# Performance work log

Measured on AMD Instinct MI355X. Metric: run time of the kernel, lower is better.

## Reference

```python
import jax, jax.numpy as jnp
import numpy as np

B, S, DIM, H = 8, 1024, 1024, 16
HID = 512  # FeedForward default hidden_dim=512 (module passes only dim)
DH = DIM // H
EPS = 1e-5


def setup_inputs() -> dict:
    key = jax.random.key(0)
    ks = jax.random.split(key, 12)
    s = 1.0 / np.sqrt(DIM)
    return {
        "x": jax.random.normal(ks[0], (B, S, DIM), dtype=jnp.float32),
        "Wq": jax.random.normal(ks[1], (DIM, DIM), dtype=jnp.float32) * s,
        "Wk": jax.random.normal(ks[2], (DIM, DIM), dtype=jnp.float32) * s,
        "Wv": jax.random.normal(ks[3], (DIM, DIM), dtype=jnp.float32) * s,
        "Wo": jax.random.normal(ks[4], (DIM, DIM), dtype=jnp.float32) * s,
        "ln1_g": jnp.ones((DIM,), jnp.float32),
        "ln1_b": jnp.zeros((DIM,), jnp.float32),
        "W1": jax.random.normal(ks[5], (DIM, HID), dtype=jnp.float32) * s,
        "b1": jnp.zeros((HID,), jnp.float32),
        "W2": jax.random.normal(ks[6], (HID, DIM), dtype=jnp.float32) * (1.0 / np.sqrt(HID)),
        "b2": jnp.zeros((DIM,), jnp.float32),
        "ln2_g": jnp.ones((DIM,), jnp.float32),
        "ln2_b": jnp.zeros((DIM,), jnp.float32),
    }


def _layer_norm(x, g, b):
    mu = jnp.mean(x, axis=-1, keepdims=True)
    var = jnp.mean(jnp.square(x - mu), axis=-1, keepdims=True)
    return (x - mu) * jax.lax.rsqrt(var + EPS) * g + b


def reference(x, Wq, Wk, Wv, Wo, ln1_g, ln1_b, W1, b1, W2, b2, ln2_g, ln2_b):
    # Multi-head self-attention (dropout = identity at eval)
    def heads(t):  # [B,S,DIM] -> [B,H,S,DH]
        return t.reshape(B, S, H, DH).transpose(0, 2, 1, 3)

    q = heads(x @ Wq)
    k = heads(x @ Wk)
    v = heads(x @ Wv)
    scores = jnp.einsum("bhqd,bhkd->bhqk", q, k) / jnp.sqrt(jnp.float32(DH))
    attn = jax.nn.softmax(scores, axis=-1)
    ctx = jnp.einsum("bhqk,bhkd->bhqd", attn, v)
    ctx = ctx.transpose(0, 2, 1, 3).reshape(B, S, DIM)
    mha = ctx @ Wo

    h = _layer_norm(mha + x, ln1_g, ln1_b)
    ff = jax.nn.relu(h @ W1 + b1) @ W2 + b2
    out = _layer_norm(ff + h, ln2_g, ln2_b)
    return out
```

## Files before the change

### kernel.cpp

```cpp
#include <hip/hip_runtime.h>
#include <cstdint>
#include <cstddef>

#define DEV __device__ __forceinline__

typedef __bf16 bf16x8 __attribute__((ext_vector_type(8)));
typedef __bf16 bf16x4 __attribute__((ext_vector_type(4)));
typedef short  short4v __attribute__((ext_vector_type(4)));
typedef float  f32x4  __attribute__((ext_vector_type(4)));

static constexpr int Bb  = 8;
static constexpr int S   = 1024;
static constexpr int DIM = 1024;
static constexpr int H   = 16;
static constexpr int DH  = 64;
static constexpr int HID = 512;
static constexpr int M   = Bb * S;

DEV uint16_t f2bf(float f) {
  union { float f; uint32_t u; } v; v.f = f;
  uint32_t r = v.u + 0x7fffu + ((v.u >> 16) & 1u);
  return (uint16_t)(r >> 16);
}
DEV float bf2f(uint32_t u) {
  union { uint32_t u; float f; } v; v.u = u << 16;
  return v.f;
}

DEV void gl_lds16(const uint16_t* g, uint16_t* lds) {
  __builtin_amdgcn_global_load_lds(
      (const __attribute__((address_space(1))) void*)g,
      (__attribute__((address_space(3))) void*)lds, 16, 0, 0);
}

DEV bf16x8 ld8(const uint16_t* p) { return *reinterpret_cast<const bf16x8*>(p); }

#if __has_builtin(__builtin_amdgcn_mfma_f32_16x16x16bf16_1k)
DEV f32x4 mfma16(bf16x4 a, bf16x4 b, f32x4 c) {
  return __builtin_amdgcn_mfma_f32_16x16x16bf16_1k(
      __builtin_bit_cast(short4v, a), __builtin_bit_cast(short4v, b), c, 0, 0, 0);
}
#else
DEV f32x4 mfma16(bf16x4 a, bf16x4 b, f32x4 c) {
  asm volatile("v_mfma_f32_16x16x16_bf16 %0, %1, %2, %0" : "+v"(c) : "v"(a), "v"(b));
  return c;
}
#endif

DEV int swz(int row, int col) {
  return row * 64 + (((col >> 3) ^ (row & 7)) << 3) + (col & 7);
}

__global__ __launch_bounds__(256) void prep_all(const float* __restrict__ x,
                                                uint16_t* __restrict__ x16,
                                                const float* __restrict__ Wq,
                                                const float* __restrict__ Wk,
                                                const float* __restrict__ Wv,
                                                const float* __restrict__ Wo,
                                                const float* __restrict__ W1,
                                                const float* __restrict__ W2,
                                                uint16_t* __restrict__ wqkv_t,
                                                uint16_t* __restrict__ wo_t,
                                                uint16_t* __restrict__ w1_t,
                                                uint16_t* __restrict__ w2_t) {
  int bid = blockIdx.x;
  int tid = threadIdx.x;
  if (bid < 4096) {
    int i = (bid * 256 + tid) * 8;
    const float4* p = reinterpret_cast<const float4*>(x + i);
    float4 a = p[0], b = p[1];
    uint4 pk;
    pk.x = (uint32_t)f2bf(a.x) | ((uint32_t)f2bf(a.y) << 16);
    pk.y = (uint32_t)f2bf(a.z) | ((uint32_t)f2bf(a.w) << 16);
    pk.z = (uint32_t)f2bf(b.x) | ((uint32_t)f2bf(b.y) << 16);
    pk.w = (uint32_t)f2bf(b.z) | ((uint32_t)f2bf(b.w) << 16);
    *reinterpret_cast<uint4*>(x16 + i) = pk;
    return;
  }
  bid -= 4096;
  const float* src;
  uint16_t* dst;
  int R, C, bx, by;
  if (bid < 4096) {
    int which = bid >> 10, id = bid & 1023;
    if (which == 0)      { src = Wq; dst = wqkv_t; }
    else if (which == 1) { src = Wk; dst = wqkv_t + 1048576; }
    else if (which == 2) { src = Wv; dst = wqkv_t + 2097152; }
    else                 { src = Wo; dst = wo_t; }
    R = 1024; C = 1024; bx = id & 31; by = id >> 5;
  } else if (bid < 4608) {
    int id = bid - 4096;
    src = W1; dst = w1_t; R = 1024; C = 512; bx = id & 15; by = id >> 4;
  } else {
    int id = bid - 4608;
    src = W2; dst = w2_t; R = 512; C = 1024; bx = id & 31; by = id >> 5;
  }
  __shared__ float tile[32][33];
  int c0 = bx * 32, r0 = by * 32;
  int tx = tid & 31, ty = tid >> 5;
  #pragma unroll
  for (int i = 0; i < 4; i++)
    tile[ty + i * 8][tx] = src[(size_t)(r0 + ty + i * 8) * C + c0 + tx];
  __syncthreads();
  #pragma unroll
  for (int i = 0; i < 4; i++)
    dst[(size_t)(c0 + ty + i * 8) * R + r0 + tx] = f2bf(tile[tx][ty + i * 8]);
}

__global__ __launch_bounds__(256) void vtrans(const uint16_t* __restrict__ qkv,
                                              uint16_t* __restrict__ vt) {
  int bh = blockIdx.x;
  int s0 = blockIdx.y * 64;
  int b = bh >> 4, h = bh & 15;
  int tid = threadIdx.x;
  __shared__ uint16_t t[64][65];
  #pragma unroll
  for (int j = 0; j < 16; j++) {
    int lin = j * 256 + tid;
    int sl = lin >> 6, d = lin & 63;
    t[d][sl] = qkv[(size_t)(b * S + s0 + sl) * 3072 + 2048 + h * 64 + d];
  }
  __syncthreads();
  #pragma unroll
  for (int j = 0; j < 16; j++) {
    int lin = j * 256 + tid;
    int dl = lin >> 6, sl = lin & 63;
    vt[((size_t)bh * 64 + dl) * S + s0 + sl] = t[dl][sl];
  }
}

template <int BIAS, int RELU, int OUT_BF16>
__global__ __launch_bounds__(256) void gemm_bt(const uint16_t* __restrict__ A,
                                               const uint16_t* __restrict__ Bt,
                                               const float* __restrict__ bias,
                                               void* __restrict__ Cout,
                                               int Mm, int N, int K) {
  __shared__ __align__(16) uint16_t As[128 * 32];
  __shared__ __align__(16) uint16_t Bs[128 * 32];
  const int tid = threadIdx.x;
  const int w = tid >> 6, l = tid & 63;
  int nwg = gridDim.x * gridDim.y;
  int lin = blockIdx.y * gridDim.x + blockIdx.x;
  if (!(nwg & 7)) lin = (lin & 7) * (nwg >> 3) + (lin >> 3);
  const int bx = lin % gridDim.x, by = lin / gridDim.x;
  const int m0 = by * 128, n0 = bx * 128;
  const int wr = (w >> 1) * 64, wc = (w & 1) * 64;
  const int wbase = w * 64;
  f32x4 acc[4][4] = {};
  const uint16_t* Ag = A + (size_t)m0 * K;
  const uint16_t* Bg = Bt + (size_t)n0 * K;

  for (int k0 = 0; k0 < K; k0 += 32) {
    __syncthreads();
    #pragma unroll
    for (int n = 0; n < 2; n++) {
      int lin2 = n * 256 + tid;
      int row = lin2 >> 2, col = (lin2 & 3) * 8;
      gl_lds16(Ag + (size_t)row * K + k0 + col, &As[(size_t)(n * 256 + wbase) * 8]);
      gl_lds16(Bg + (size_t)row * K + k0 + col, &Bs[(size_t)(n * 256 + wbase) * 8]);
    }
    __syncthreads();
    bf16x8 af[4], bfr[4];
    #pragma unroll
    for (int i = 0; i < 4; i++) {
      af[i]  = ld8(&As[(wr + i * 16 + (l & 15)) * 32 + (l >> 4) * 8]);
      bfr[i] = ld8(&Bs[(wc + i * 16 + (l & 15)) * 32 + (l >> 4) * 8]);
    }
    #pragma unroll
    for (int i = 0; i < 4; i++)
      #pragma unroll
      for (int j = 0; j < 4; j++)
        acc[i][j] = __builtin_amdgcn_mfma_f32_16x16x32_bf16(af[i], bfr[j], acc[i][j], 0, 0, 0);
  }

  const int r0 = m0 + wr + (l >> 4) * 4;
  const int c0 = n0 + wc + (l & 15);
  #pragma unroll
  for (int j = 0; j < 4; j++) {
    int col = c0 + j * 16;
    float bv = BIAS ? bias[col] : 0.0f;
    #pragma unroll
    for (int i = 0; i < 4; i++) {
      #pragma unroll
      for (int r = 0; r < 4; r++) {
        float v = acc[i][j][r] + bv;
        if (RELU) v = fmaxf(v, 0.0f);
        int row = r0 + i * 16 + r;
        if (OUT_BF16)
          ((uint16_t*)Cout)[(size_t)row * N + col] = f2bf(v);
        else
          ((float*)Cout)[(size_t)row * N + col] = v;
      }
    }
  }
}

__global__ __launch_bounds__(512, 2) void gemm256(const uint16_t* __restrict__ A,
                                                  const uint16_t* __restrict__ Bt,
                                                  uint16_t* __restrict__ Cout,
                                                  int N, int K) {
  __shared__ __align__(16) uint16_t As[2][256 * 64];
  __shared__ __align__(16) uint16_t Bs[2][256 * 64];
  const int tid = threadIdx.x;
  const int w = tid >> 6, l = tid & 63;
  const int hi = l >> 4, c = l & 15;
  int nwg = gridDim.x * gridDim.y;
  int lin = blockIdx.y * gridDim.x + blockIdx.x;
  if (!(nwg & 7)) lin = (lin & 7) * (nwg >> 3) + (lin >> 3);
  const int bx = lin % gridDim.x, by = lin / gridDim.x;
  const int m0 = by * 256, n0 = bx * 256;
  const int wr = w >> 2, wc = w & 3;
  const uint16_t* Ag = A + (size_t)m0 * K;
  const uint16_t* Bg = Bt + (size_t)n0 * K;
  f32x4 acc[8][4] = {};

  const int srow = tid >> 3, sch = tid & 7;
  auto stage = [&](int k0, int buf) {
    #pragma unroll
    for (int i = 0; i < 4; i++) {
      int row = i * 64 + srow;
      int scol = (sch ^ (row & 7)) * 8;
      gl_lds16(Ag + (size_t)row * K + k0 + scol, &As[buf][(i * 512 + w * 64) * 8]);
    }
    #pragma unroll
    for (int i = 0; i < 4; i++) {
      int row = i * 64 + srow;
      int scol = (sch ^ (row & 7)) * 8;
      gl_lds16(Bg + (size_t)row * K + k0 + scol, &Bs[buf][(i * 512 + w * 64) * 8]);
    }
  };

  stage(0, 0);
  stage(64, 1);
  asm volatile("s_waitcnt vmcnt(8)" ::: "memory");
  __builtin_amdgcn_s_barrier();

  const int NTK = K >> 6;
  for (int t = 0; t < NTK; t++) {
    const int cur = t & 1;
    const uint16_t* Ab = As[cur];
    const uint16_t* Bb = Bs[cur];
    bf16x8 bfr[4][2];
    #pragma unroll
    for (int ni = 0; ni < 4; ni++)
      #pragma unroll
      for (int kk = 0; kk < 2; kk++)
        bfr[ni][kk] = ld8(&Bb[swz(wc * 64 + ni * 16 + c, kk * 32 + hi * 8)]);
    #pragma unroll
    for (int mi = 0; mi < 8; mi++) {
      bf16x8 a0 = ld8(&Ab[swz(wr * 128 + mi * 16 + c, hi * 8)]);
      bf16x8 a1 = ld8(&Ab[swz(wr * 128 + mi * 16 + c, 32 + hi * 8)]);
      #pragma unroll
      for (int ni = 0; ni < 4; ni++) {
        acc[mi][ni] = __builtin_amdgcn_mfma_f32_16x16x32_bf16(a0, bfr[ni][0], acc[mi][ni], 0, 0, 0);
        acc[mi][ni] = __builtin_amdgcn_mfma_f32_16x16x32_bf16(a1, bfr[ni][1], acc[mi][ni], 0, 0, 0);
      }
    }
    if (t == NTK - 1) break;
    asm volatile("s_waitcnt lgkmcnt(0)" ::: "memory");
    __builtin_amdgcn_s_barrier();
    if (t + 2 < NTK) {
      stage((t + 2) << 6, cur);
      asm volatile("s_waitcnt vmcnt(8)" ::: "memory");
    } else {
      asm volatile("s_waitcnt vmcnt(0)" ::: "memory");
    }
    __builtin_amdgcn_s_barrier();
  }

  const int r0 = m0 + wr * 128 + hi * 4;
  const int c0 = n0 + wc * 64 + c;
  #pragma unroll
  for (int mi = 0; mi < 8; mi++)
    #pragma unroll
    for (int ni = 0; ni < 4; ni++)
      #pragma unroll
      for (int r = 0; r < 4; r++)
        Cout[(size_t)(r0 + mi * 16 + r) * N + c0 + ni * 16] = f2bf(acc[mi][ni][r]);
}

__global__ __launch_bounds__(256, 4) void attn8(const uint16_t* __restrict__ qkv,
                                                const uint16_t* __restrict__ vt,
                                                uint16_t* __restrict__ ctx) {
  int blk = blockIdx.x;
  int xcd = blk & 7, idx = blk >> 3;
  int qt = idx & 7;
  int bh = xcd + 8 * (idx >> 3);
  int h = bh & 15, b = bh >> 4;
  int q0 = qt * 128;
  int tid = threadIdx.x;
  int w = tid >> 6, l = tid & 63;
  int hi = l >> 4, c = l & 15;

  __shared__ __align__(16) uint16_t Klds[2][64 * 64];
  __shared__ __align__(16) uint16_t Vlds[2][64 * 64];

  const uint16_t* qbase = qkv + (size_t)(b * S + q0 + w * 32) * 3072 + h * 64;
  bf16x8 aq[2][2];
  #pragma unroll
  for (int qg = 0; qg < 2; qg++)
    #pragma unroll
    for (int dk = 0; dk < 2; dk++)
      aq[qg][dk] = ld8(qbase + (size_t)(qg * 16 + c) * 3072 + dk * 32 + hi * 8);

  f32x4 acc[2][4] = {};
  float psum[2] = {};

  const uint16_t* kgbase = qkv + (size_t)(b * S) * 3072 + 1024 + h * 64;
  const uint16_t* vgbase = vt + (size_t)(b * 16 + h) * 64 * S;

  int srow = tid >> 3, sch = tid & 7;
  uint4 kreg[2], vreg[2];

  auto load_tiles = [&](int kt) {
    #pragma unroll
    for (int i = 0; i < 2; i++) {
      int row = srow + i * 32;
      kreg[i] = *(const uint4*)(kgbase + (size_t)(kt + row) * 3072 + sch * 8);
      vreg[i] = *(const uint4*)(vgbase + (size_t)row * S + kt + sch * 8);
    }
  };
  auto store_tiles = [&](int buf) {
    #pragma unroll
    for (int i = 0; i < 2; i++) {
      int row = srow + i * 32;
      *(uint4*)&Klds[buf][swz(row, sch * 8)] = kreg[i];
      *(uint4*)&Vlds[buf][swz(row, sch * 8)] = vreg[i];
    }
  };

  load_tiles(0);
  store_tiles(0);
  __syncthreads();

  constexpr float C2 = 0.125f * 1.44269504f;
  constexpr int NT = S / 64;
  for (int t = 0; t < NT; t++) {
    int cur = t & 1;
    if (t + 1 < NT) load_tiles((t + 1) * 64);

    #pragma unroll
    for (int kb = 0; kb < 4; kb++) {
      bf16x8 kf0 = ld8(&Klds[cur][swz(kb * 16 + c, hi * 8)]);
      bf16x8 kf1 = ld8(&Klds[cur][swz(kb * 16 + c, 32 + hi * 8)]);
      bf16x4 pb[2];
      #pragma unroll
      for (int qg = 0; qg < 2; qg++) {
        f32x4 z = {0.f, 0.f, 0.f, 0.f};
        z = __builtin_amdgcn_mfma_f32_16x16x32_bf16(kf0, aq[qg][0], z, 0, 0, 0);
        z = __builtin_amdgcn_mfma_f32_16x16x32_bf16(kf1, aq[qg][1], z, 0, 0, 0);
        #pragma unroll
        for (int r = 0; r < 4; r++) {
          float p = exp2f(z[r] * C2);
          psum[qg] += p;
          pb[qg][r] = (__bf16)p;
        }
      }
      #pragma unroll
      for (int db = 0; db < 4; db++) {
        bf16x4 va = *(const bf16x4*)&Vlds[cur][swz(db * 16 + c, kb * 16 + hi * 4)];
        acc[0][db] = mfma16(va, pb[0], acc[0][db]);
        acc[1][db] = mfma16(va, pb[1], acc[1][db]);
      }
    }

    if (t + 1 < NT) store_tiles(cur ^ 1);
    __syncthreads();
  }

  #pragma unroll
  for (int qg = 0; qg < 2; qg++) {
    psum[qg] += __shfl_xor(psum[qg], 16);
    psum[qg] += __shfl_xor(psum[qg], 32);
  }

  uint16_t* Bw = &Vlds[w >> 1][(w & 1) * 2048];
  #pragma unroll
  for (int qg = 0; qg < 2; qg++) {
    float inv = 1.0f / psum[qg];
    int q = qg * 16 + c;
    #pragma unroll
    for (int db = 0; db < 4; db++) {
      uint2 pk;
      pk.x = (uint32_t)f2bf(acc[qg][db][0] * inv) |
             ((uint32_t)f2bf(acc[qg][db][1] * inv) << 16);
      pk.y = (uint32_t)f2bf(acc[qg][db][2] * inv) |
             ((uint32_t)f2bf(acc[qg][db][3] * inv) << 16);
      int chunk4 = (db * 4 + hi) ^ (q & 15);
      *(uint2*)&Bw[q * 64 + chunk4 * 4] = pk;
    }
  }
  int rrow = l >> 3, rch = l & 7;
  size_t gq0 = (size_t)(b * S + q0 + w * 32);
  #pragma unroll
  for (int it = 0; it < 4; it++) {
    int row = it * 8 + rrow;
    int k0 = (2 * rch) ^ (row & 15);
    int base = (k0 & ~1) * 4;
    uint4 v = *(const uint4*)&Bw[row * 64 + base];
    if (row & 1) { uint32_t t0 = v.x, t1 = v.y; v.x = v.z; v.y = v.w; v.z = t0; v.w = t1; }
    *(uint4*)&ctx[(gq0 + row) * DIM + h * 64 + rch * 8] = v;
  }
}

__global__ __launch_bounds__(256) void ln1_b(const uint16_t* __restrict__ a16,
                                             const uint16_t* __restrict__ x16,
                                             const float* __restrict__ g,
                                             const float* __restrict__ beta,
                                             uint16_t* __restrict__ h16) {
  int row = blockIdx.x;
  int t = threadIdx.x;
  int w = t >> 6, l = t & 63;
  uint2 av = reinterpret_cast<const uint2*>(a16 + (size_t)row * DIM)[t];
  uint2 xv = reinterpret_cast<const uint2*>(x16 + (size_t)row * DIM)[t];
  float v0 = bf2f(av.x & 0xffff) + bf2f(xv.x & 0xffff);
  float v1 = bf2f(av.x >> 16)    + bf2f(xv.x >> 16);
  float v2 = bf2f(av.y & 0xffff) + bf2f(xv.y & 0xffff);
  float v3 = bf2f(av.y >> 16)    + bf2f(xv.y >> 16);
  float s = v0 + v1 + v2 + v3;
  float sq = v0 * v0 + v1 * v1 + v2 * v2 + v3 * v3;
  #pragma unroll
  for (int off = 32; off >= 1; off >>= 1) {
    s += __shfl_xor(s, off);
    sq += __shfl_xor(sq, off);
  }
  __shared__ float ws[4], wq[4];
  if (l == 0) { ws[w] = s; wq[w] = sq; }
  __syncthreads();
  s = ws[0] + ws[1] + ws[2] + ws[3];
  sq = wq[0] + wq[1] + wq[2] + wq[3];
  float mu = s * (1.0f / DIM);
  float var = sq * (1.0f / DIM) - mu * mu;
  float rstd = rsqrtf(var + 1e-5f);
  const float4 gv = reinterpret_cast<const float4*>(g)[t];
  const float4 btv = reinterpret_cast<const float4*>(beta)[t];
  float o0 = (v0 - mu) * rstd * gv.x + btv.x;
  float o1 = (v1 - mu) * rstd * gv.y + btv.y;
  float o2 = (v2 - mu) * rstd * gv.z + btv.z;
  float o3 = (v3 - mu) * rstd * gv.w + btv.w;
  uint2 pk;
  pk.x = (uint32_t)f2bf(o0) | ((uint32_t)f2bf(o1) << 16);
  pk.y = (uint32_t)f2bf(o2) | ((uint32_t)f2bf(o3) << 16);
  reinterpret_cast<uint2*>(h16 + (size_t)row * DIM)[t] = pk;
}

__global__ __launch_bounds__(256) void ln2_b(const uint16_t* __restrict__ ff16,
                                             const uint16_t* __restrict__ h16,
                                             const float* __restrict__ g,
                                             const float* __restrict__ beta,
                                             float* __restrict__ out_f) {
  int row = blockIdx.x;
  int t = threadIdx.x;
  int w = t >> 6, l = t & 63;
  uint2 av = reinterpret_cast<const uint2*>(ff16 + (size_t)row * DIM)[t];
  uint2 hv = reinterpret_cast<const uint2*>(h16 + (size_t)row * DIM)[t];
  float v0 = bf2f(av.x & 0xffff) + bf2f(hv.x & 0xffff);
  float v1 = bf2f(av.x >> 16)    + bf2f(hv.x >> 16);
  float v2 = bf2f(av.y & 0xffff) + bf2f(hv.y & 0xffff);
  float v3 = bf2f(av.y >> 16)    + bf2f(hv.y >> 16);
  float s = v0 + v1 + v2 + v3;
  float sq = v0 * v0 + v1 * v1 + v2 * v2 + v3 * v3;
  #pragma unroll
  for (int off = 32; off >= 1; off >>= 1) {
    s += __shfl_xor(s, off);
    sq += __shfl_xor(sq, off);
  }
  __shared__ float ws[4], wq[4];
  if (l == 0) { ws[w] = s; wq[w] = sq; }
  __syncthreads();
  s = ws[0] + ws[1] + ws[2] + ws[3];
  sq = wq[0] + wq[1] + wq[2] + wq[3];
  float mu = s * (1.0f / DIM);
  float var = sq * (1.0f / DIM) - mu * mu;
  float rstd = rsqrtf(var + 1e-5f);
  const float4 gv = reinterpret_cast<const float4*>(g)[t];
  const float4 btv = reinterpret_cast<const float4*>(beta)[t];
  float4 o;
  o.x = (v0 - mu) * rstd * gv.x + btv.x;
  o.y = (v1 - mu) * rstd * gv.y + btv.y;
  o.z = (v2 - mu) * rstd * gv.z + btv.z;
  o.w = (v3 - mu) * rstd * gv.w + btv.w;
  reinterpret_cast<float4*>(out_f + (size_t)row * DIM)[t] = o;
}

extern "C" void kernel_launch(void* const* d_in, const int* in_sizes, int n_in,
                              void* d_out, int out_size, void* d_ws, size_t ws_size,
                              hipStream_t stream) {
  const float* x    = (const float*)d_in[0];
  const float* Wq   = (const float*)d_in[1];
  const float* Wk   = (const float*)d_in[2];
  const float* Wv   = (const float*)d_in[3];
  const float* Wo   = (const float*)d_in[4];
  const float* ln1g = (const float*)d_in[5];
  const float* ln1b = (const float*)d_in[6];
  const float* W1   = (const float*)d_in[7];
  const float* b1   = (const float*)d_in[8];
  const float* W2   = (const float*)d_in[9];
  const float* b2   = (const float*)d_in[10];
  const float* ln2g = (const float*)d_in[11];
  const float* ln2b = (const float*)d_in[12];
  float* out = (float*)d_out;

  char* ws = (char*)d_ws;
  uint16_t* wqkv_t = (uint16_t*)(ws + 0);
  uint16_t* wo_t   = (uint16_t*)(ws + 6291456);
  uint16_t* w1_t   = (uint16_t*)(ws + 8388608);
  uint16_t* w2_t   = (uint16_t*)(ws + 9437184);
  uint16_t* x16    = (uint16_t*)(ws + 10485760);
  uint16_t* qkv16  = (uint16_t*)(ws + 27262976);
  uint16_t* mha16  = (uint16_t*)(ws + 27262976);
  uint16_t* ff16   = (uint16_t*)(ws + 27262976);
  uint16_t* h16    = (uint16_t*)(ws + 60817408);
  uint16_t* vt16   = (uint16_t*)(ws + 77594624);
  uint16_t* mid16  = vt16;
  uint16_t* ctx16  = (uint16_t*)(ws + 94371840);

  prep_all<<<9216, 256, 0, stream>>>(x, x16, Wq, Wk, Wv, Wo, W1, W2,
                                     wqkv_t, wo_t, w1_t, w2_t);
  gemm256<<<dim3(12, 32), 512, 0, stream>>>(x16, wqkv_t, qkv16, 3072, DIM);
  vtrans<<<dim3(128, 16), 256, 0, stream>>>(qkv16, vt16);
  attn8<<<1024, 256, 0, stream>>>(qkv16, vt16, ctx16);
  gemm_bt<0, 0, 1><<<dim3(8, 64), 256, 0, stream>>>(ctx16, wo_t, nullptr, mha16, M, DIM, DIM);
  ln1_b<<<M, 256, 0, stream>>>(mha16, x16, ln1g, ln1b, h16);
  gemm_bt<1, 1, 1><<<dim3(4, 64), 256, 0, stream>>>(h16, w1_t, b1, mid16, M, HID, DIM);
  gemm_bt<1, 0, 1><<<dim3(8, 64), 256, 0, stream>>>(mid16, w2_t, b2, ff16, M, DIM, HID);
  ln2_b<<<M, 256, 0, stream>>>(ff16, h16, ln2g, ln2b, out);
}
```

Baseline: 262.4 us.

## Fuse V transpose into QKV GEMM epilogue and stage attention tiles directly to LDS

The QKV GEMM epilogue now writes the V columns straight into a per-head transposed layout (vt), which removes the separate vtrans kernel and its extra read and write of V. The attention kernel switches from register-staged K/V loads plus LDS stores to direct global-to-LDS loads (gl_lds16) with an XOR column swizzle, then waits on vmcnt before each barrier. This saves one launch, V memory traffic and VGPR pressure. In exchange the transposed stores are narrower and strided, and waiting for the loads at the end of each iteration may reduce the overlap between loads and compute.

```diff
diff --git a/kernel.cpp b/kernel.cpp
--- a/kernel.cpp
+++ b/kernel.cpp
@@ -107,28 +107,6 @@
     dst[(size_t)(c0 + ty + i * 8) * R + r0 + tx] = f2bf(tile[tx][ty + i * 8]);
 }
 
-__global__ __launch_bounds__(256) void vtrans(const uint16_t* __restrict__ qkv,
-                                              uint16_t* __restrict__ vt) {
-  int bh = blockIdx.x;
-  int s0 = blockIdx.y * 64;
-  int b = bh >> 4, h = bh & 15;
-  int tid = threadIdx.x;
-  __shared__ uint16_t t[64][65];
-  #pragma unroll
-  for (int j = 0; j < 16; j++) {
-    int lin = j * 256 + tid;
-    int sl = lin >> 6, d = lin & 63;
-    t[d][sl] = qkv[(size_t)(b * S + s0 + sl) * 3072 + 2048 + h * 64 + d];
-  }
-  __syncthreads();
-  #pragma unroll
-  for (int j = 0; j < 16; j++) {
-    int lin = j * 256 + tid;
-    int dl = lin >> 6, sl = lin & 63;
-    vt[((size_t)bh * 64 + dl) * S + s0 + sl] = t[dl][sl];
-  }
-}
-
 template <int BIAS, int RELU, int OUT_BF16>
 __global__ __launch_bounds__(256) void gemm_bt(const uint16_t* __restrict__ A,
                                                const uint16_t* __restrict__ Bt,
@@ -198,6 +176,7 @@
 __global__ __launch_bounds__(512, 2) void gemm256(const uint16_t* __restrict__ A,
                                                   const uint16_t* __restrict__ Bt,
                                                   uint16_t* __restrict__ Cout,
+                                                  uint16_t* __restrict__ vt,
                                                   int N, int K) {
   __shared__ __align__(16) uint16_t As[2][256 * 64];
   __shared__ __align__(16) uint16_t Bs[2][256 * 64];
@@ -270,16 +249,32 @@
 
   const int r0 = m0 + wr * 128 + hi * 4;
   const int c0 = n0 + wc * 64 + c;
-  #pragma unroll
-  for (int mi = 0; mi < 8; mi++)
-    #pragma unroll
-    for (int ni = 0; ni < 4; ni++)
-      #pragma unroll
-      for (int r = 0; r < 4; r++)
-        Cout[(size_t)(r0 + mi * 16 + r) * N + c0 + ni * 16] = f2bf(acc[mi][ni][r]);
-}
-
-__global__ __launch_bounds__(256, 4) void attn8(const uint16_t* __restrict__ qkv,
+  if (c0 >= 2048) {
+    #pragma unroll
+    for (int ni = 0; ni < 4; ni++) {
+      int hd = c0 + ni * 16 - 2048;
+      #pragma unroll
+      for (int mi = 0; mi < 8; mi++) {
+        int row = r0 + mi * 16;
+        size_t vi = ((size_t)(row >> 10) * 1024 + hd) * 1024 + (row & 1023);
+        uint2 pk;
+        pk.x = (uint32_t)f2bf(acc[mi][ni][0]) | ((uint32_t)f2bf(acc[mi][ni][1]) << 16);
+        pk.y = (uint32_t)f2bf(acc[mi][ni][2]) | ((uint32_t)f2bf(acc[mi][ni][3]) << 16);
+        *(uint2*)&vt[vi] = pk;
+      }
+    }
+  } else {
+    #pragma unroll
+    for (int mi = 0; mi < 8; mi++)
+      #pragma unroll
+      for (int ni = 0; ni < 4; ni++)
+        #pragma unroll
+        for (int r = 0; r < 4; r++)
+          Cout[(size_t)(r0 + mi * 16 + r) * N + c0 + ni * 16] = f2bf(acc[mi][ni][r]);
+  }
+}
+
+__global__ __launch_bounds__(256, 4) void attn9(const uint16_t* __restrict__ qkv,
                                                 const uint16_t* __restrict__ vt,
                                                 uint16_t* __restrict__ ctx) {
   int blk = blockIdx.x;
@@ -309,35 +304,28 @@
   const uint16_t* kgbase = qkv + (size_t)(b * S) * 3072 + 1024 + h * 64;
   const uint16_t* vgbase = vt + (size_t)(b * 16 + h) * 64 * S;
 
-  int srow = tid >> 3, sch = tid & 7;
-  uint4 kreg[2], vreg[2];
-
-  auto load_tiles = [&](int kt) {
+  const int lr = l >> 3, lc = l & 7;
+  const int scol = (lc ^ lr) * 8;
+  auto stage = [&](int kt, int buf) {
     #pragma unroll
     for (int i = 0; i < 2; i++) {
-      int row = srow + i * 32;
-      kreg[i] = *(const uint4*)(kgbase + (size_t)(kt + row) * 3072 + sch * 8);
-      vreg[i] = *(const uint4*)(vgbase + (size_t)row * S + kt + sch * 8);
+      int slab = w * 2 + i;
+      gl_lds16(kgbase + (size_t)(kt + slab * 8 + lr) * 3072 + scol,
+               &Klds[buf][slab * 512]);
+      gl_lds16(vgbase + (size_t)(slab * 8 + lr) * S + kt + scol,
+               &Vlds[buf][slab * 512]);
     }
   };
-  auto store_tiles = [&](int buf) {
-    #pragma unroll
-    for (int i = 0; i < 2; i++) {
-      int row = srow + i * 32;
-      *(uint4*)&Klds[buf][swz(row, sch * 8)] = kreg[i];
-      *(uint4*)&Vlds[buf][swz(row, sch * 8)] = vreg[i];
-    }
-  };
-
-  load_tiles(0);
-  store_tiles(0);
+
+  stage(0, 0);
+  asm volatile("s_waitcnt vmcnt(0)" ::: "memory");
   __syncthreads();
 
   constexpr float C2 = 0.125f * 1.44269504f;
   constexpr int NT = S / 64;
   for (int t = 0; t < NT; t++) {
     int cur = t & 1;
-    if (t + 1 < NT) load_tiles((t + 1) * 64);
+    if (t + 1 < NT) stage((t + 1) * 64, cur ^ 1);
 
     #pragma unroll
     for (int kb = 0; kb < 4; kb++) {
@@ -364,7 +352,7 @@
       }
     }
 
-    if (t + 1 < NT) store_tiles(cur ^ 1);
+    asm volatile("s_waitcnt vmcnt(0)" ::: "memory");
     __syncthreads();
   }
 
@@ -517,9 +505,8 @@
 
   prep_all<<<9216, 256, 0, stream>>>(x, x16, Wq, Wk, Wv, Wo, W1, W2,
                                      wqkv_t, wo_t, w1_t, w2_t);
-  gemm256<<<dim3(12, 32), 512, 0, stream>>>(x16, wqkv_t, qkv16, 3072, DIM);
-  vtrans<<<dim3(128, 16), 256, 0, stream>>>(qkv16, vt16);
-  attn8<<<1024, 256, 0, stream>>>(qkv16, vt16, ctx16);
+  gemm256<<<dim3(12, 32), 512, 0, stream>>>(x16, wqkv_t, qkv16, vt16, 3072, DIM);
+  attn9<<<1024, 256, 0, stream>>>(qkv16, vt16, ctx16);
   gemm_bt<0, 0, 1><<<dim3(8, 64), 256, 0, stream>>>(ctx16, wo_t, nullptr, mha16, M, DIM, DIM);
   ln1_b<<<M, 256, 0, stream>>>(mha16, x16, ln1g, ln1b, h16);
   gemm_bt<1, 1, 1><<<dim3(4, 64), 256, 0, stream>>>(h16, w1_t, b1, mid16, M, HID, DIM);
```

New measurement: 243.6 us. 1.08x faster.
